# Kernel tuning notes

Measured on AMD Instinct MI355X. Metric: run time of the kernel, lower is better.

Reference implementation:

```python
import jax, jax.numpy as jnp
import numpy as np

B = 100000   # batch of nodes
K = 10       # sampled neighbours per node
N = 1000000  # total nodes in feature table
D = 128      # feature dim


def setup_inputs() -> dict:
    key = jax.random.key(0)
    k1, k2, k3 = jax.random.split(key, 3)
    nodes = jax.random.randint(k1, (B,), 0, N, dtype=jnp.int64)
    neighbours = jax.random.randint(k2, (B, K), 0, N, dtype=jnp.int64)
    features = jax.random.normal(k3, (N, D), dtype=jnp.float32)
    return {"nodes": nodes, "neighbours": neighbours, "features": features}


def reference(nodes, neighbours, features):
    # Neighborhood = sampled neighbours union self node -> [B, K+1]
    neigh_idx = jnp.concatenate([neighbours, nodes[:, None]], axis=1)
    # Gather features: [B, K+1, D] (irregular memory-bound gather)
    gathered = features[neigh_idx]
    # Row-normalized mask matmul == mean over the neighborhood axis
    return gathered.mean(axis=1)  # [B, D]
```

## Files before the change

kernel.cpp:

```cpp
#include <hip/hip_runtime.h>


#define KNEIGH 10
#define DDIM 128

__global__ __launch_bounds__(256) void MeanAggregator_36386962932386_kernel(
    const int* __restrict__ nodes,
    const int* __restrict__ neighbours,
    const float* __restrict__ features,
    float* __restrict__ out,
    int B)
{
    const int node = blockIdx.x * 8 + (threadIdx.x >> 5);
    if (node >= B) return;
    const int c = threadIdx.x & 31;

    int idx[KNEIGH + 1];
    const long long nb = (long long)node * KNEIGH;
#pragma unroll
    for (int j = 0; j < KNEIGH; ++j) idx[j] = neighbours[nb + j];
    idx[KNEIGH] = nodes[node];

    float4 v[KNEIGH + 1];
#pragma unroll
    for (int j = 0; j < KNEIGH + 1; ++j) {
        v[j] = ((const float4*)(features + (long long)idx[j] * DDIM))[c];
    }

    float4 acc = v[0];
#pragma unroll
    for (int j = 1; j < KNEIGH + 1; ++j) {
        acc.x += v[j].x;
        acc.y += v[j].y;
        acc.z += v[j].z;
        acc.w += v[j].w;
    }

    const float s = 1.0f / (float)(KNEIGH + 1);
    acc.x *= s; acc.y *= s; acc.z *= s; acc.w *= s;

    ((float4*)(out + (long long)node * DDIM))[c] = acc;
}

extern "C" void kernel_launch(void* const* d_in, const int* in_sizes, int n_in,
                              void* d_out, int out_size, void* d_ws, size_t ws_size,
                              hipStream_t stream)
{
    const int* nodes      = (const int*)d_in[0];
    const int* neighbours = (const int*)d_in[1];
    const float* features = (const float*)d_in[2];
    float* out            = (float*)d_out;

    const int B = in_sizes[0];
    const int blocks = (B + 7) / 8;

    MeanAggregator_36386962932386_kernel<<<blocks, 256, 0, stream>>>(
        nodes, neighbours, features, out, B);
}
```

Measured before the change: 651.6 us.

## Use grid-stride persistent loop with prefetched next indices and nontemporal stores

Replaces the one-node-per-group launch with a 2048-block grid-stride loop. While the feature rows for the current node are being gathered, each group also loads the neighbour indices for its next node, which hides index-load latency. Output is written with nontemporal stores so it does not pollute the cache used by the gather. The risk is lower occupancy and less memory-level parallelism from the smaller grid.

```diff
diff --git a/kernel.cpp b/kernel.cpp
--- a/kernel.cpp
+++ b/kernel.cpp
@@ -3,6 +3,8 @@
 
 #define KNEIGH 10
 #define DDIM 128
+
+typedef float v4f __attribute__((ext_vector_type(4)));
 
 __global__ __launch_bounds__(256) void MeanAggregator_36386962932386_kernel(
     const int* __restrict__ nodes,
@@ -11,35 +13,50 @@
     float* __restrict__ out,
     int B)
 {
-    const int node = blockIdx.x * 8 + (threadIdx.x >> 5);
+    const int g = threadIdx.x >> 5;
+    const int c = threadIdx.x & 31;
+    const int step = gridDim.x * 8;
+
+    int node = blockIdx.x * 8 + g;
     if (node >= B) return;
-    const int c = threadIdx.x & 31;
 
     int idx[KNEIGH + 1];
-    const long long nb = (long long)node * KNEIGH;
+    {
+        const long long nb = (long long)node * KNEIGH;
 #pragma unroll
-    for (int j = 0; j < KNEIGH; ++j) idx[j] = neighbours[nb + j];
-    idx[KNEIGH] = nodes[node];
-
-    float4 v[KNEIGH + 1];
-#pragma unroll
-    for (int j = 0; j < KNEIGH + 1; ++j) {
-        v[j] = ((const float4*)(features + (long long)idx[j] * DDIM))[c];
+        for (int j = 0; j < KNEIGH; ++j) idx[j] = neighbours[nb + j];
+        idx[KNEIGH] = nodes[node];
     }
 
-    float4 acc = v[0];
+    while (true) {
+        const int next = node + step;
+
+        v4f v[KNEIGH + 1];
 #pragma unroll
-    for (int j = 1; j < KNEIGH + 1; ++j) {
-        acc.x += v[j].x;
-        acc.y += v[j].y;
-        acc.z += v[j].z;
-        acc.w += v[j].w;
+        for (int j = 0; j <= KNEIGH; ++j) {
+            v[j] = ((const v4f*)(features + (long long)idx[j] * DDIM))[c];
+        }
+
+        int nidx[KNEIGH + 1];
+        if (next < B) {
+            const long long nb2 = (long long)next * KNEIGH;
+#pragma unroll
+            for (int j = 0; j < KNEIGH; ++j) nidx[j] = neighbours[nb2 + j];
+            nidx[KNEIGH] = nodes[next];
+        }
+
+        v4f acc = v[0];
+#pragma unroll
+        for (int j = 1; j <= KNEIGH; ++j) acc += v[j];
+        acc *= (1.0f / (float)(KNEIGH + 1));
+
+        __builtin_nontemporal_store(acc, (v4f*)(out + (long long)node * DDIM) + c);
+
+        if (next >= B) break;
+        node = next;
+#pragma unroll
+        for (int j = 0; j <= KNEIGH; ++j) idx[j] = nidx[j];
     }
-
-    const float s = 1.0f / (float)(KNEIGH + 1);
-    acc.x *= s; acc.y *= s; acc.z *= s; acc.w *= s;
-
-    ((float4*)(out + (long long)node * DDIM))[c] = acc;
 }
 
 extern "C" void kernel_launch(void* const* d_in, const int* in_sizes, int n_in,
@@ -52,7 +69,10 @@
     float* out            = (float*)d_out;
 
     const int B = in_sizes[0];
-    const int blocks = (B + 7) / 8;
+
+    int blocks = 2048;
+    const int max_blocks = (B + 7) / 8;
+    if (blocks > max_blocks) blocks = max_blocks;
 
     MeanAggregator_36386962932386_kernel<<<blocks, 256, 0, stream>>>(
         nodes, neighbours, features, out, B);
```

New measurement: 653.7 us. Within noise of the previous version (+0.3%).
